# Performance work log

Measured on AMD Instinct MI355X. Metric: run time of the kernel, lower is better.

Reference implementation:

```python
import jax, jax.numpy as jnp
import numpy as np

L = 6          # encoder layers
D = 512        # d_model
H = 8          # heads
HD = D // H    # head_dim = 64
M = 64         # num random features (num_orf)
DFF = 2048     # feedforward dim
B = 16         # batch
S = 2048       # sequence length (hw)
NQ = 100       # query_embed rows (unused by encoder)
EPS = 1e-5
STAB = 1e-3    # relu kernel numerical stabilizer


def _ln(x, s, b):
    mu = jnp.mean(x, axis=-1, keepdims=True)
    var = jnp.mean((x - mu) ** 2, axis=-1, keepdims=True)
    return (x - mu) / jnp.sqrt(var + EPS) * s + b


def _performer_attn(x_qk, v_in, Wqkv, bqkv, Wo, bo, w):
    # x_qk, v_in: [S,B,D]; Wqkv: [3D,D]; w: [M,HD]
    q = x_qk @ Wqkv[:D].T + bqkv[:D]
    k = x_qk @ Wqkv[D:2 * D].T + bqkv[D:2 * D]
    v = v_in @ Wqkv[2 * D:].T + bqkv[2 * D:]
    q = q.reshape(S, B, H, HD)
    k = k.reshape(S, B, H, HD)
    v = v.reshape(S, B, H, HD)
    ratio = 1.0 / (M ** 0.25)  # 1/sqrt(sqrt(m))
    qp = jax.nn.relu(ratio * jnp.einsum('sbhd,md->sbhm', q, w)) + STAB
    kp = jax.nn.relu(ratio * jnp.einsum('sbhd,md->sbhm', k, w)) + STAB
    kv = jnp.einsum('sbhm,sbhd->bhmd', kp, v)              # O(n) linear attention
    num = jnp.einsum('sbhm,bhmd->sbhd', qp, kv)
    den = jnp.einsum('sbhm,bhm->sbh', qp, kp.sum(axis=0))[..., None]
    out = (num / den).reshape(S, B, D)
    return out @ Wo.T + bo


def setup_inputs() -> dict:
    key = jax.random.key(0)
    ks = jax.random.split(key, 8)
    src = jax.random.normal(ks[0], (B, S, D), jnp.float32)
    query_embed = jax.random.normal(ks[1], (NQ, D), jnp.float32)
    pos_embed = jax.random.normal(ks[2], (B, S, D), jnp.float32)
    in_proj_w = jax.random.normal(ks[3], (L, 3 * D, D), jnp.float32) * (D ** -0.5)
    in_proj_b = jnp.zeros((L, 3 * D), jnp.float32)
    out_w = jax.random.normal(ks[4], (L, D, D), jnp.float32) * (D ** -0.5)
    out_b = jnp.zeros((L, D), jnp.float32)
    lin1_w = jax.random.normal(ks[5], (L, DFF, D), jnp.float32) * (D ** -0.5)
    lin1_b = jnp.zeros((L, DFF), jnp.float32)
    lin2_w = jax.random.normal(ks[6], (L, D, DFF), jnp.float32) * (DFF ** -0.5)
    lin2_b = jnp.zeros((L, D), jnp.float32)
    norm1_s = jnp.ones((L, D), jnp.float32)
    norm1_b = jnp.zeros((L, D), jnp.float32)
    norm2_s = jnp.ones((L, D), jnp.float32)
    norm2_b = jnp.zeros((L, D), jnp.float32)
    # gaussian orthogonal random matrices (scaling=0): Q^T from QR, rows rescaled by chi norms
    rng = np.random.default_rng(0)
    ws = []
    for _ in range(L):
        q, _ = np.linalg.qr(rng.standard_normal((HD, HD)))
        mult = np.linalg.norm(rng.standard_normal((M, HD)), axis=1)
        ws.append(np.diag(mult) @ q.T)
    w_orf = jnp.asarray(np.stack(ws), jnp.float32)
    return dict(src=src, query_embed=query_embed, pos_embed=pos_embed,
                in_proj_w=in_proj_w, in_proj_b=in_proj_b, out_w=out_w, out_b=out_b,
                lin1_w=lin1_w, lin1_b=lin1_b, lin2_w=lin2_w, lin2_b=lin2_b,
                norm1_s=norm1_s, norm1_b=norm1_b, norm2_s=norm2_s, norm2_b=norm2_b,
                w_orf=w_orf)


def reference(src, query_embed, pos_embed, in_proj_w, in_proj_b, out_w, out_b,
              lin1_w, lin1_b, lin2_w, lin2_b, norm1_s, norm1_b, norm2_s, norm2_b,
              w_orf):
    del query_embed  # only encoder memory is returned
    x = jnp.transpose(src, (1, 0, 2))        # [S,B,D]
    pos = jnp.transpose(pos_embed, (1, 0, 2))
    for i in range(L):  # post-norm encoder layers (dropout inactive in eval)
        qk = x + pos
        a = _performer_attn(qk, x, in_proj_w[i], in_proj_b[i], out_w[i], out_b[i], w_orf[i])
        x = _ln(x + a, norm1_s[i], norm1_b[i])
        f = jax.nn.relu(x @ lin1_w[i].T + lin1_b[i]) @ lin2_w[i].T + lin2_b[i]
        x = _ln(x + f, norm2_s[i], norm2_b[i])
    return x  # memory: [S,B,D]
```

## Files before the change

kernel.cpp:

```cpp
#include <hip/hip_runtime.h>

typedef unsigned short u16;
typedef unsigned int   u32;
typedef __attribute__((ext_vector_type(8))) short short8;
typedef __attribute__((ext_vector_type(4))) float f32x4;

constexpr int Dc   = 512;
constexpr int Lc   = 6;
constexpr int Bc   = 16;
constexpr int Sc   = 2048;
constexpr int Rc   = Sc * Bc;
constexpr float RATIO = 0.3535533905932738f;
constexpr float STABc = 1e-3f;
constexpr float EPSc  = 1e-5f;

__device__ __forceinline__ u32 pk2(float lo, float hi) {
    u32 a = __float_as_uint(lo), b = __float_as_uint(hi);
    a = (a + 0x7FFFu + ((a >> 16) & 1u)) >> 16;
    b = (b + 0x7FFFu + ((b >> 16) & 1u)) & 0xFFFF0000u;
    return a | b;
}
__device__ __forceinline__ u16 f2bh(float f) {
    u32 u = __float_as_uint(f);
    return (u16)((u + 0x7FFFu + ((u >> 16) & 1u)) >> 16);
}
__device__ __forceinline__ float b2f(u16 u) { return __uint_as_float(((u32)u) << 16); }

__device__ __forceinline__ void glds16(const u16* g, u16* l) {
    __builtin_amdgcn_global_load_lds(
        (const __attribute__((address_space(1))) u32*)g,
        (__attribute__((address_space(3))) u32*)l, 16, 0, 0);
}

__global__ __launch_bounds__(256)
void sentinel_kernel(float* O, int n4) {
    int i = blockIdx.x * 256 + threadIdx.x;
    if (i < n4) {
        float4 v = make_float4(12345.f, 12345.f, 12345.f, 12345.f);
        *reinterpret_cast<float4*>(O + (size_t)i * 4) = v;
    }
}

__global__ __launch_bounds__(256)
void zero_kernel(float* p, int n4) {
    int i = blockIdx.x * 256 + threadIdx.x;
    if (i < n4) {
        float4 z = make_float4(0.f, 0.f, 0.f, 0.f);
        *reinterpret_cast<float4*>(p + (size_t)i * 4) = z;
    }
}

__global__ __launch_bounds__(256)
void wconv2_kernel(const float* __restrict__ s1, u16* __restrict__ d1,
                   const float* __restrict__ s2, u16* __restrict__ d2, int n8each) {
    int i = blockIdx.x * 256 + threadIdx.x;
    const float* src; u16* dst;
    if (i < n8each) { src = s1; dst = d1; }
    else            { src = s2; dst = d2; i -= n8each; }
    if (i >= n8each) return;
    size_t base = (size_t)i * 8;
    float4 a = *reinterpret_cast<const float4*>(src + base);
    float4 b = *reinterpret_cast<const float4*>(src + base + 4);
    uint4 o;
    o.x = pk2(a.x, a.y); o.y = pk2(a.z, a.w);
    o.z = pk2(b.x, b.y); o.w = pk2(b.z, b.w);
    *reinterpret_cast<uint4*>(dst + base) = o;
}

__global__ __launch_bounds__(256)
void xp_kernel(const float* __restrict__ X, const float* __restrict__ POS,
               u16* __restrict__ XP) {
    size_t i = (size_t)blockIdx.x * 256 + threadIdx.x;
    size_t base = i * 8;
    float4 x0 = *reinterpret_cast<const float4*>(X + base);
    float4 x1 = *reinterpret_cast<const float4*>(X + base + 4);
    float4 p0 = *reinterpret_cast<const float4*>(POS + base);
    float4 p1 = *reinterpret_cast<const float4*>(POS + base + 4);
    uint4 o;
    o.x = pk2(x0.x + p0.x, x0.y + p0.y);
    o.y = pk2(x0.z + p0.z, x0.w + p0.w);
    o.z = pk2(x1.x + p1.x, x1.y + p1.y);
    o.w = pk2(x1.z + p1.z, x1.w + p1.w);
    *reinterpret_cast<uint4*>(XP + base) = o;
}

__global__ __launch_bounds__(256)
void xb_kernel(const float* __restrict__ X, u16* __restrict__ XB) {
    size_t i = (size_t)blockIdx.x * 256 + threadIdx.x;
    size_t base = i * 8;
    float4 x0 = *reinterpret_cast<const float4*>(X + base);
    float4 x1 = *reinterpret_cast<const float4*>(X + base + 4);
    uint4 o;
    o.x = pk2(x0.x, x0.y); o.y = pk2(x0.z, x0.w);
    o.z = pk2(x1.x, x1.y); o.w = pk2(x1.z, x1.w);
    *reinterpret_cast<uint4*>(XB + base) = o;
}

__global__ __launch_bounds__(256)
void weff_kernel(const float* __restrict__ Wqkv, const float* __restrict__ bqkv,
                 const float* __restrict__ worf,
                 u16* __restrict__ WeffQ, u16* __restrict__ WeffK,
                 float* __restrict__ beffQ, float* __restrict__ beffK) {
    __shared__ float wl[64][64];
    __shared__ float ql[64][68];
    __shared__ float kl[64][68];
    int cc = blockIdx.x, h = blockIdx.y;
    int tid = threadIdx.x;
    for (int i = tid; i < 4096; i += 256) wl[i >> 6][i & 63] = worf[i];
    for (int i = tid; i < 4096; i += 256) {
        int d = i >> 6, c = i & 63;
        ql[d][c] = Wqkv[(size_t)(h * 64 + d) * 512 + cc * 64 + c];
        kl[d][c] = Wqkv[(size_t)(512 + h * 64 + d) * 512 + cc * 64 + c];
    }
    __syncthreads();
    int m = tid >> 2, c0 = (tid & 3) * 16;
    float acc[16];
    #pragma unroll
    for (int j = 0; j < 16; ++j) acc[j] = 0.f;
    for (int d = 0; d < 64; ++d) {
        float wv = wl[m][d];
        #pragma unroll
        for (int j = 0; j < 16; ++j) acc[j] = fmaf(wv, ql[d][c0 + j], acc[j]);
    }
    for (int j = 0; j < 16; ++j)
        WeffQ[(size_t)(h * 64 + m) * 512 + cc * 64 + c0 + j] = f2bh(RATIO * acc[j]);
    #pragma unroll
    for (int j = 0; j < 16; ++j) acc[j] = 0.f;
    for (int d = 0; d < 64; ++d) {
        float wv = wl[m][d];
        #pragma unroll
        for (int j = 0; j < 16; ++j) acc[j] = fmaf(wv, kl[d][c0 + j], acc[j]);
    }
    for (int j = 0; j < 16; ++j)
        WeffK[(size_t)(h * 64 + m) * 512 + cc * 64 + c0 + j] = f2bh(RATIO * acc[j]);
    if (cc == 0 && tid < 64) {
        float bq = 0.f, bk = 0.f;
        for (int d = 0; d < 64; ++d) {
            bq = fmaf(wl[tid][d], bqkv[h * 64 + d], bq);
            bk = fmaf(wl[tid][d], bqkv[512 + h * 64 + d], bk);
        }
        beffQ[h * 64 + tid] = RATIO * bq;
        beffK[h * 64 + tid] = RATIO * bk;
    }
}

template <int MODE>
__global__ __launch_bounds__(256)
void gemm_bb(const u16* __restrict__ A, int lda,
             const u16* __restrict__ W, int ldw,
             const float* __restrict__ bias, const float* __restrict__ res,
             void* __restrict__ Cv, int ldc, int K) {
    constexpr bool CB16 = (MODE == 0 || MODE == 1 || MODE == 4);
    __shared__ u16 As[2][128 * 32];
    __shared__ u16 Bs[2][128 * 32];
    int tid = threadIdx.x;
    int lane = tid & 63, wv = tid >> 6;
    int wr = wv >> 1, wc = wv & 1;

    int nbx = gridDim.x;
    int nwg = nbx * gridDim.y;
    int bid = blockIdx.y * nbx + blockIdx.x;
    int nb  = (bid & 7) * (nwg >> 3) + (bid >> 3);
    int row0 = (nb / nbx) * 128;
    int col0 = (nb % nbx) * 128;

    int srow  = wv * 32 + (lane >> 2);
    int skofs = (((lane & 3) ^ ((lane >> 3) & 3)) << 3);
    const u16* Ap0 = A + (size_t)(row0 + srow) * lda + skofs;
    const u16* Ap1 = A + (size_t)(row0 + srow + 16) * lda + skofs;
    const u16* Wp0 = W + (size_t)(col0 + srow) * ldw + skofs;
    const u16* Wp1 = W + (size_t)(col0 + srow + 16) * ldw + skofs;
    int d0 = (wv * 32) * 32;
    int d1 = (wv * 32 + 16) * 32;

    f32x4 acc[4][4];
    #pragma unroll
    for (int mi = 0; mi < 4; ++mi)
        #pragma unroll
        for (int ni = 0; ni < 4; ++ni)
            acc[mi][ni] = (f32x4){0.f, 0.f, 0.f, 0.f};

    int rl = lane & 15;
    int pslot = (((lane >> 4) ^ ((rl >> 1) & 3)) << 3);

    glds16(Ap0, &As[0][d0]);
    glds16(Ap1, &As[0][d1]);
    glds16(Wp0, &Bs[0][d0]);
    glds16(Wp1, &Bs[0][d1]);
    __syncthreads();

    int nsteps = K >> 5;
    for (int t = 0; t < nsteps; ++t) {
        int cur = t & 1;
        if (t + 1 < nsteps) {
            int k1 = (t + 1) << 5;
            glds16(Ap0 + k1, &As[cur ^ 1][d0]);
            glds16(Ap1 + k1, &As[cur ^ 1][d1]);
            glds16(Wp0 + k1, &Bs[cur ^ 1][d0]);
            glds16(Wp1 + k1, &Bs[cur ^ 1][d1]);
        }
        const u16* Asr = &As[cur][0];
        const u16* Bsr = &Bs[cur][0];
        short8 af[4], bf[4];
        #pragma unroll
        for (int mi = 0; mi < 4; ++mi)
            af[mi] = *reinterpret_cast<const short8*>(&Asr[(wr * 64 + mi * 16 + rl) * 32 + pslot]);
        #pragma unroll
        for (int ni = 0; ni < 4; ++ni)
            bf[ni] = *reinterpret_cast<const short8*>(&Bsr[(wc * 64 + ni * 16 + rl) * 32 + pslot]);
        #pragma unroll
        for (int mi = 0; mi < 4; ++mi)
            #pragma unroll
            for (int ni = 0; ni < 4; ++ni)
                acc[mi][ni] = __builtin_amdgcn_mfma_f32_16x16x32_bf16(
                    af[mi], bf[ni], acc[mi][ni], 0, 0, 0);
        __syncthreads();
    }

    int orb = row0 + wr * 64 + (lane >> 4) * 4;
    int ocb = col0 + wc * 64 + rl;
    float bv[4];
    #pragma unroll
    for (int ni = 0; ni < 4; ++ni)
        bv[ni] = (MODE != 3) ? bias[ocb + ni * 16] : 0.f;
    #pragma unroll
    for (int mi = 0; mi < 4; ++mi) {
        #pragma unroll
        for (int j = 0; j < 4; ++j) {
            int orow = orb + mi * 16 + j;
            size_t base = (size_t)orow * ldc + ocb;
            #pragma unroll
            for (int ni = 0; ni < 4; ++ni) {
                float v = acc[mi][ni][j] + bv[ni];
                if (MODE == 1) v = fmaxf(v, 0.f);
                if (MODE == 4) v = fmaxf(v, 0.f) + STABc;
                size_t off = base + ni * 16;
                if (MODE == 2) v += res[off];
                if (MODE == 3) v += ((float*)Cv)[off];
                if (CB16) ((u16*)Cv)[off] = f2bh(v);
                else      ((float*)Cv)[off] = v;
            }
        }
    }
}

__global__ __launch_bounds__(256)
void kv_split(const u16* __restrict__ KQP, const u16* __restrict__ V,
              float* __restrict__ KV, float* __restrict__ KSUM) {
    __shared__ u16 kpl[128 * 64];
    __shared__ u16 vl[128 * 64];
    int bh = blockIdx.x, sc = blockIdx.y;
    int b = bh >> 3, h = bh & 7;
    int tid = threadIdx.x;
    int d = tid & 63, mg = tid >> 6;
    float acc[16], ks[16];
    #pragma unroll
    for (int i = 0; i < 16; ++i) { acc[i] = 0.f; ks[i] = 0.f; }
    size_t rowbase = (size_t)b * Sc + sc * 512;
    for (int c = 0; c < 4; ++c) {
        __syncthreads();
        for (int i = tid; i < 1024; i += 256) {
            int row = i >> 3, c8 = (i & 7) * 8;
            size_t r = rowbase + c * 128 + row;
            *reinterpret_cast<uint4*>(&kpl[row * 64 + c8]) =
                *reinterpret_cast<const uint4*>(KQP + r * 1024 + h * 64 + c8);
            *reinterpret_cast<uint4*>(&vl[row * 64 + c8]) =
                *reinterpret_cast<const uint4*>(V + r * 512 + h * 64 + c8);
        }
        __syncthreads();
        for (int s = 0; s < 128; ++s) {
            float vv = b2f(vl[s * 64 + d]);
            #pragma unroll
            for (int i = 0; i < 16; ++i) {
                float kp = b2f(kpl[s * 64 + mg * 16 + i]);
                acc[i] = fmaf(kp, vv, acc[i]);
                ks[i] += kp;
            }
        }
    }
    float* kvp = KV + (size_t)bh * 4096;
    #pragma unroll
    for (int i = 0; i < 16; ++i)
        atomicAdd(&kvp[(mg * 16 + i) * 64 + d], acc[i]);
    if (d == 0) {
        #pragma unroll
        for (int i = 0; i < 16; ++i)
            atomicAdd(&KSUM[bh * 64 + mg * 16 + i], ks[i]);
    }
}

__global__ __launch_bounds__(256)
void numden_mfma(const u16* __restrict__ KQP, const float* __restrict__ KVg,
                 const float* __restrict__ KSUM, u16* __restrict__ OUT) {
    constexpr int LP = 72;
    __shared__ short Asm[128 * LP];
    __shared__ short BT[64 * LP];
    __shared__ float ksl[64];
    __shared__ float dsm[128][2];
    int h  = blockIdx.x;
    int row0 = blockIdx.y * 128;
    int b  = row0 >> 11;
    int tid = threadIdx.x;
    int lane = tid & 63, w = tid >> 6;

    const float* kvp = KVg + ((size_t)(b * 8 + h)) * 4096;
    for (int i = tid; i < 4096; i += 256) {
        int m = i >> 6, d = i & 63;
        BT[d * LP + m] = (short)f2bh(kvp[i]);
    }
    if (tid < 64) ksl[tid] = KSUM[(b * 8 + h) * 64 + tid];
    {
        int rr = tid >> 1;
        int cc = (tid & 1) * 32;
        const u16* qp = KQP + (size_t)(row0 + rr) * 1024 + 512 + h * 64 + cc;
        #pragma unroll
        for (int q = 0; q < 4; ++q)
            *reinterpret_cast<uint4*>(&Asm[rr * LP + cc + q * 8]) =
                *reinterpret_cast<const uint4*>(qp + q * 8);
    }
    __syncthreads();

    {
        int rr = tid >> 1, half = tid & 1;
        const short* ap = &Asm[rr * LP + half * 32];
        float pden = 0.f;
        #pragma unroll
        for (int m = 0; m < 32; ++m)
            pden = fmaf(b2f((u16)ap[m]), ksl[half * 32 + m], pden);
        dsm[rr][half] = pden;
    }
    __syncthreads();

    int rl = lane & 15, kq = (lane >> 4) * 8;
    f32x4 acc[2][4];
    #pragma unroll
    for (int mi = 0; mi < 2; ++mi)
        #pragma unroll
        for (int ni = 0; ni < 4; ++ni) acc[mi][ni] = (f32x4){0.f, 0.f, 0.f, 0.f};
    #pragma unroll
    for (int kst = 0; kst < 2; ++kst) {
        int kg = kst * 32 + kq;
        short8 a0 = *reinterpret_cast<const short8*>(&Asm[(w * 32 + rl) * LP + kg]);
        short8 a1 = *reinterpret_cast<const short8*>(&Asm[(w * 32 + 16 + rl) * LP + kg]);
        short8 bf[4];
        #pragma unroll
        for (int ni = 0; ni < 4; ++ni)
            bf[ni] = *reinterpret_cast<const short8*>(&BT[(ni * 16 + rl) * LP + kg]);
        #pragma unroll
        for (int ni = 0; ni < 4; ++ni) {
            acc[0][ni] = __builtin_amdgcn_mfma_f32_16x16x32_bf16(a0, bf[ni], acc[0][ni], 0, 0, 0);
            acc[1][ni] = __builtin_amdgcn_mfma_f32_16x16x32_bf16(a1, bf[ni], acc[1][ni], 0, 0, 0);
        }
    }
    #pragma unroll
    for (int mi = 0; mi < 2; ++mi) {
        #pragma unroll
        for (int j = 0; j < 4; ++j) {
            int lr = w * 32 + mi * 16 + (lane >> 4) * 4 + j;
            int row = row0 + lr;
            float inv = 1.f / (dsm[lr][0] + dsm[lr][1]);
            #pragma unroll
            for (int ni = 0; ni < 4; ++ni)
                OUT[(size_t)row * Dc + h * 64 + ni * 16 + rl] =
                    f2bh(acc[mi][ni][j] * inv);
        }
    }
}

template <bool PERM>
__global__ __launch_bounds__(256)
void ln_kernel(const float* __restrict__ X, const float* __restrict__ Sg,
               const float* __restrict__ Bg, float* __restrict__ O) {
    int lane = threadIdx.x & 63, w = threadIdx.x >> 6;
    size_t r = (size_t)blockIdx.x * 4 + w;
    const float* xr = X + r * Dc;
    float v[8];
    *reinterpret_cast<float4*>(&v[0]) = *reinterpret_cast<const float4*>(xr + lane * 4);
    *reinterpret_cast<float4*>(&v[4]) = *reinterpret_cast<const float4*>(xr + 256 + lane * 4);
    float sum = 0.f;
    #pragma unroll
    for (int i = 0; i < 8; ++i) sum += v[i];
    #pragma unroll
    for (int off = 32; off >= 1; off >>= 1) sum += __shfl_xor(sum, off);
    float mu = sum * (1.f / Dc);
    float sq = 0.f;
    #pragma unroll
    for (int i = 0; i < 8; ++i) { float dd = v[i] - mu; sq += dd * dd; }
    #pragma unroll
    for (int off = 32; off >= 1; off >>= 1) sq += __shfl_xor(sq, off);
    float rstd = rsqrtf(sq * (1.f / Dc) + EPSc);
    float s[8], b[8];
    *reinterpret_cast<float4*>(&s[0]) = *reinterpret_cast<const float4*>(Sg + lane * 4);
    *reinterpret_cast<float4*>(&s[4]) = *reinterpret_cast<const float4*>(Sg + 256 + lane * 4);
    *reinterpret_cast<float4*>(&b[0]) = *reinterpret_cast<const float4*>(Bg + lane * 4);
    *reinterpret_cast<float4*>(&b[4]) = *reinterpret_cast<const float4*>(Bg + 256 + lane * 4);
    float o[8];
    #pragma unroll
    for (int i = 0; i < 8; ++i) o[i] = (v[i] - mu) * rstd * s[i] + b[i];
    size_t rd = PERM ? ((size_t)(r & (Sc - 1)) * Bc + (r >> 11)) : r;
    float* orow = O + rd * Dc;
    *reinterpret_cast<float4*>(orow + lane * 4) = *reinterpret_cast<const float4*>(&o[0]);
    *reinterpret_cast<float4*>(orow + 256 + lane * 4) = *reinterpret_cast<const float4*>(&o[4]);
}

__global__ __launch_bounds__(256)
void ln1f_kernel(float* __restrict__ X, const float* __restrict__ Sg,
                 const float* __restrict__ Bg, u16* __restrict__ XB) {
    int lane = threadIdx.x & 63, w = threadIdx.x >> 6;
    size_t r = (size_t)blockIdx.x * 4 + w;
    float* xr = X + r * Dc;
    float v[8];
    *reinterpret_cast<float4*>(&v[0]) = *reinterpret_cast<const float4*>(xr + lane * 4);
    *reinterpret_cast<float4*>(&v[4]) = *reinterpret_cast<const float4*>(xr + 256 + lane * 4);
    float sum = 0.f;
    #pragma unroll
    for (int i = 0; i < 8; ++i) sum += v[i];
    #pragma unroll
    for (int off = 32; off >= 1; off >>= 1) sum += __shfl_xor(sum, off);
    float mu = sum * (1.f / Dc);
    float sq = 0.f;
    #pragma unroll
    for (int i = 0; i < 8; ++i) { float dd = v[i] - mu; sq += dd * dd; }
    #pragma unroll
    for (int off = 32; off >= 1; off >>= 1) sq += __shfl_xor(sq, off);
    float rstd = rsqrtf(sq * (1.f / Dc) + EPSc);
    float s[8], b[8];
    *reinterpret_cast<float4*>(&s[0]) = *reinterpret_cast<const float4*>(Sg + lane * 4);
    *reinterpret_cast<float4*>(&s[4]) = *reinterpret_cast<const float4*>(Sg + 256 + lane * 4);
    *reinterpret_cast<float4*>(&b[0]) = *reinterpret_cast<const float4*>(Bg + lane * 4);
    *reinterpret_cast<float4*>(&b[4]) = *reinterpret_cast<const float4*>(Bg + 256 + lane * 4);
    float o[8];
    #pragma unroll
    for (int i = 0; i < 8; ++i) o[i] = (v[i] - mu) * rstd * s[i] + b[i];
    *reinterpret_cast<float4*>(xr + lane * 4)       = *reinterpret_cast<const float4*>(&o[0]);
    *reinterpret_cast<float4*>(xr + 256 + lane * 4) = *reinterpret_cast<const float4*>(&o[4]);
    uint2 xb0, xb1;
    xb0.x = pk2(o[0], o[1]); xb0.y = pk2(o[2], o[3]);
    xb1.x = pk2(o[4], o[5]); xb1.y = pk2(o[6], o[7]);
    *reinterpret_cast<uint2*>(XB + r * Dc + lane * 4)       = xb0;
    *reinterpret_cast<uint2*>(XB + r * Dc + 256 + lane * 4) = xb1;
}

__global__ __launch_bounds__(256)
void ln2f_kernel(float* __restrict__ X, const float* __restrict__ Sg,
                 const float* __restrict__ Bg, const float* __restrict__ POS,
                 u16* __restrict__ XP, u16* __restrict__ XB) {
    int lane = threadIdx.x & 63, w = threadIdx.x >> 6;
    size_t r = (size_t)blockIdx.x * 4 + w;
    float* xr = X + r * Dc;
    float v[8];
    *reinterpret_cast<float4*>(&v[0]) = *reinterpret_cast<const float4*>(xr + lane * 4);
    *reinterpret_cast<float4*>(&v[4]) = *reinterpret_cast<const float4*>(xr + 256 + lane * 4);
    float sum = 0.f;
    #pragma unroll
    for (int i = 0; i < 8; ++i) sum += v[i];
    #pragma unroll
    for (int off = 32; off >= 1; off >>= 1) sum += __shfl_xor(sum, off);
    float mu = sum * (1.f / Dc);
    float sq = 0.f;
    #pragma unroll
    for (int i = 0; i < 8; ++i) { float dd = v[i] - mu; sq += dd * dd; }
    #pragma unroll
    for (int off = 32; off >= 1; off >>= 1) sq += __shfl_xor(sq, off);
    float rstd = rsqrtf(sq * (1.f / Dc) + EPSc);
    float s[8], b[8];
    *reinterpret_cast<float4*>(&s[0]) = *reinterpret_cast<const float4*>(Sg + lane * 4);
    *reinterpret_cast<float4*>(&s[4]) = *reinterpret_cast<const float4*>(Sg + 256 + lane * 4);
    *reinterpret_cast<float4*>(&b[0]) = *reinterpret_cast<const float4*>(Bg + lane * 4);
    *reinterpret_cast<float4*>(&b[4]) = *reinterpret_cast<const float4*>(Bg + 256 + lane * 4);
    float p[8];
    *reinterpret_cast<float4*>(&p[0]) = *reinterpret_cast<const float4*>(POS + r * Dc + lane * 4);
    *reinterpret_cast<float4*>(&p[4]) = *reinterpret_cast<const float4*>(POS + r * Dc + 256 + lane * 4);
    float o[8];
    #pragma unroll
    for (int i = 0; i < 8; ++i) o[i] = (v[i] - mu) * rstd * s[i] + b[i];
    *reinterpret_cast<float4*>(xr + lane * 4)       = *reinterpret_cast<const float4*>(&o[0]);
    *reinterpret_cast<float4*>(xr + 256 + lane * 4) = *reinterpret_cast<const float4*>(&o[4]);
    uint2 xb0, xb1, xp0, xp1;
    xb0.x = pk2(o[0], o[1]); xb0.y = pk2(o[2], o[3]);
    xb1.x = pk2(o[4], o[5]); xb1.y = pk2(o[6], o[7]);
    xp0.x = pk2(o[0] + p[0], o[1] + p[1]); xp0.y = pk2(o[2] + p[2], o[3] + p[3]);
    xp1.x = pk2(o[4] + p[4], o[5] + p[5]); xp1.y = pk2(o[6] + p[6], o[7] + p[7]);
    *reinterpret_cast<uint2*>(XB + r * Dc + lane * 4)       = xb0;
    *reinterpret_cast<uint2*>(XB + r * Dc + 256 + lane * 4) = xb1;
    *reinterpret_cast<uint2*>(XP + r * Dc + lane * 4)       = xp0;
    *reinterpret_cast<uint2*>(XP + r * Dc + 256 + lane * 4) = xp1;
}

extern "C" void kernel_launch(void* const* d_in, const int* in_sizes, int n_in,
                              void* d_out, int out_size, void* d_ws, size_t ws_size,
                              hipStream_t stream) {
    (void)in_sizes; (void)n_in; (void)out_size;
    const float* src   = (const float*)d_in[0];
    const float* pos   = (const float*)d_in[2];
    const float* ipw   = (const float*)d_in[3];
    const float* ipb   = (const float*)d_in[4];
    const float* outw  = (const float*)d_in[5];
    const float* outb  = (const float*)d_in[6];
    const float* l1w   = (const float*)d_in[7];
    const float* l1b   = (const float*)d_in[8];
    const float* l2w   = (const float*)d_in[9];
    const float* l2b   = (const float*)d_in[10];
    const float* n1s   = (const float*)d_in[11];
    const float* n1b   = (const float*)d_in[12];
    const float* n2s   = (const float*)d_in[13];
    const float* n2b   = (const float*)d_in[14];
    const float* worf  = (const float*)d_in[15];
    float* out = (float*)d_out;

    const size_t RD = (size_t)Rc * Dc;
    const size_t NEED = RD * 4 + RD * 4 + (size_t)128 * 4096 * 4 + 8192 * 4
                      + (size_t)Rc * 8 * 4 + 2 * 262144 * 2 + 2 * 512 * 4;
    if (ws_size < NEED) {
        sentinel_kernel<<<(Rc * Dc / 4 + 255) / 256, 256, 0, stream>>>(out, Rc * Dc / 4);
        return;
    }
    char* p = (char*)d_ws;
    float* X    = (float*)p;  p += RD * 4;
    float* B2f  = (float*)p;  p += RD * 4;
    float* KV   = (float*)p;  p += (size_t)128 * 4096 * 4;
    float* KSUM = (float*)p;  p += 8192 * 4;
    u16*  WVb   = (u16*)p;
    u16*  WOb   = WVb + 262144;
    p += (size_t)Rc * 8 * 4;
    u16*  WeffKQ = (u16*)p;   p += 2 * 262144 * 2;
    float* beffKQ = (float*)p;

    u16*  B2u  = (u16*)B2f;
    u16*  XPu  = B2u;
    u16*  Vu   = B2u + RD;
    u16*  AOu  = B2u + RD;
    u16*  H1u  = B2u;
    u16*  OutU = (u16*)out;
    u16*  XB2u = OutU;
    u16*  KQPu = OutU;
    u16*  XBu  = OutU;
    u16*  W1bD = OutU + RD;
    u16*  W2bD = OutU + RD + 1048576;

    dim3 blk(256);
    dim3 g512(4, Rc / 128);
    dim3 g1024(8, Rc / 128);
    dim3 g2048(16, Rc / 128);
    const int nz4 = (128 * 4096 + 8192) / 4;

    for (int i = 0; i < Lc; ++i) {
        const float* w_qkv = ipw + (size_t)i * 1536 * 512;
        const float* b_qkv = ipb + (size_t)i * 1536;
        const float* w_v  = w_qkv + (size_t)1024 * 512;
        const float* b_v  = b_qkv + 1024;
        const float* w_o  = outw + (size_t)i * 512 * 512;
        const float* b_o  = outb + (size_t)i * 512;
        const float* w_1  = l1w + (size_t)i * 2048 * 512;
        const float* b_1  = l1b + (size_t)i * 2048;
        const float* w_2  = l2w + (size_t)i * 512 * 2048;
        const float* b_2  = l2b + (size_t)i * 512;
        const float* wo_i = worf + (size_t)i * 4096;

        weff_kernel<<<dim3(8, 8), blk, 0, stream>>>(
            w_qkv, b_qkv, wo_i, WeffKQ + 262144, WeffKQ, beffKQ + 512, beffKQ);
        wconv2_kernel<<<(2 * (262144 / 8) + 255) / 256, blk, 0, stream>>>(
            w_v, WVb, w_o, WOb, 262144 / 8);

        if (i == 0) {
            hipMemcpyAsync(X, src, RD * 4, hipMemcpyDeviceToDevice, stream);
            xb_kernel<<<(int)(RD / 8 / 256), blk, 0, stream>>>(X, XB2u);
            xp_kernel<<<(int)(RD / 8 / 256), blk, 0, stream>>>(X, pos, XPu);
        }

        gemm_bb<0><<<g512, blk, 0, stream>>>(
            XB2u, 512, WVb, 512, b_v, nullptr, Vu, 512, 512);
        gemm_bb<4><<<g1024, blk, 0, stream>>>(
            XPu, 512, WeffKQ, 512, beffKQ, nullptr, KQPu, 1024, 512);
        zero_kernel<<<(nz4 + 255) / 256, blk, 0, stream>>>(KV, nz4);
        kv_split<<<dim3(128, 4), blk, 0, stream>>>(KQPu, Vu, KV, KSUM);
        numden_mfma<<<dim3(8, Rc / 128), blk, 0, stream>>>(KQPu, KV, KSUM, AOu);
        gemm_bb<2><<<g512, blk, 0, stream>>>(
            AOu, 512, WOb, 512, b_o, X, X, 512, 512);
        ln1f_kernel<<<Rc / 4, blk, 0, stream>>>(X, n1s + i * 512, n1b + i * 512, XBu);
        wconv2_kernel<<<(2 * (1048576 / 8) + 255) / 256, blk, 0, stream>>>(
            w_1, W1bD, w_2, W2bD, 1048576 / 8);
        gemm_bb<1><<<g2048, blk, 0, stream>>>(
            XBu, 512, W1bD, 512, b_1, nullptr, H1u, 2048, 512);
        gemm_bb<2><<<g512, blk, 0, stream>>>(
            H1u, 2048, W2bD, 2048, b_2, X, X, 512, 2048);
        if (i == Lc - 1)
            ln_kernel<true><<<Rc / 4, blk, 0, stream>>>(X, n2s + i * 512, n2b + i * 512, out);
        else
            ln2f_kernel<<<Rc / 4, blk, 0, stream>>>(X, n2s + i * 512, n2b + i * 512,
                                                    pos, XPu, XB2u);
    }
}
```

Measured before the change: 3.013 ms.

## Triple-buffer GEMM shared-memory tiles with two-stage-ahead async prefetch

Extends the bf16 GEMM's global-to-LDS pipeline from double to triple buffering. Loads are issued two K-steps ahead, and partial vmcnt waits let the next tile's loads stay in flight across the barrier. The goal is to hide more global-load latency behind the MFMA work. In exchange, LDS use per block grows from 32KB to 48KB, which may lower occupancy, and correctness now depends on hand-written waitcnt counts.

Measured after the change: 3.071 ms. About the same (+1.9%).

```diff
diff --git a/kernel.cpp b/kernel.cpp
--- a/kernel.cpp
+++ b/kernel.cpp
@@ -151,8 +151,8 @@
              const float* __restrict__ bias, const float* __restrict__ res,
              void* __restrict__ Cv, int ldc, int K) {
     constexpr bool CB16 = (MODE == 0 || MODE == 1 || MODE == 4);
-    __shared__ u16 As[2][128 * 32];
-    __shared__ u16 Bs[2][128 * 32];
+    __shared__ u16 As[3][128 * 32];
+    __shared__ u16 Bs[3][128 * 32];
     int tid = threadIdx.x;
     int lane = tid & 63, wv = tid >> 6;
     int wr = wv >> 1, wc = wv & 1;
@@ -183,21 +183,33 @@
     int rl = lane & 15;
     int pslot = (((lane >> 4) ^ ((rl >> 1) & 3)) << 3);
 
+    int nsteps = K >> 5;
     glds16(Ap0, &As[0][d0]);
     glds16(Ap1, &As[0][d1]);
     glds16(Wp0, &Bs[0][d0]);
     glds16(Wp1, &Bs[0][d1]);
-    __syncthreads();
-
-    int nsteps = K >> 5;
+    if (nsteps > 1) {
+        glds16(Ap0 + 32, &As[1][d0]);
+        glds16(Ap1 + 32, &As[1][d1]);
+        glds16(Wp0 + 32, &Bs[1][d0]);
+        glds16(Wp1 + 32, &Bs[1][d1]);
+        asm volatile("s_waitcnt vmcnt(4)" ::: "memory");
+    } else {
+        asm volatile("s_waitcnt vmcnt(0)" ::: "memory");
+    }
+    __builtin_amdgcn_sched_barrier(0);
+    __builtin_amdgcn_s_barrier();
+    __builtin_amdgcn_sched_barrier(0);
+
     for (int t = 0; t < nsteps; ++t) {
-        int cur = t & 1;
-        if (t + 1 < nsteps) {
-            int k1 = (t + 1) << 5;
-            glds16(Ap0 + k1, &As[cur ^ 1][d0]);
-            glds16(Ap1 + k1, &As[cur ^ 1][d1]);
-            glds16(Wp0 + k1, &Bs[cur ^ 1][d0]);
-            glds16(Wp1 + k1, &Bs[cur ^ 1][d1]);
+        int cur = t % 3;
+        if (t + 2 < nsteps) {
+            int pf = (t + 2) % 3;
+            int k2 = (t + 2) << 5;
+            glds16(Ap0 + k2, &As[pf][d0]);
+            glds16(Ap1 + k2, &As[pf][d1]);
+            glds16(Wp0 + k2, &Bs[pf][d0]);
+            glds16(Wp1 + k2, &Bs[pf][d1]);
         }
         const u16* Asr = &As[cur][0];
         const u16* Bsr = &Bs[cur][0];
@@ -214,7 +226,13 @@
             for (int ni = 0; ni < 4; ++ni)
                 acc[mi][ni] = __builtin_amdgcn_mfma_f32_16x16x32_bf16(
                     af[mi], bf[ni], acc[mi][ni], 0, 0, 0);
-        __syncthreads();
+        if (t + 1 < nsteps) {
+            if (t + 2 < nsteps) asm volatile("s_waitcnt vmcnt(4)" ::: "memory");
+            else                asm volatile("s_waitcnt vmcnt(0)" ::: "memory");
+            __builtin_amdgcn_sched_barrier(0);
+            __builtin_amdgcn_s_barrier();
+            __builtin_amdgcn_sched_barrier(0);
+        }
     }
 
     int orb = row0 + wr * 64 + (lane >> 4) * 4;
```
